# Performance work log

Measured on AMD Instinct MI355X. Metric: run time of the kernel, lower is better.

The kernel has to match this reference:

```python
import jax, jax.numpy as jnp
import numpy as np


def setup_inputs() -> dict:
    key = jax.random.key(0)
    k1, k2, k3, k4, k5 = jax.random.split(key, 5)
    B, S, IC, OC = 4, 2048, 4096, 4096
    n_out = int(0.05 * IC)  # 204 outlier columns
    return {
        "x": jax.random.normal(k1, (B, S, IC), dtype=jnp.float32),
        "weight": jax.random.normal(k2, (OC, IC), dtype=jnp.float32) * 0.02,
        "bias": jax.random.normal(k3, (OC,), dtype=jnp.float32) * 0.02,
        "outlier_weight": jax.random.normal(k4, (OC, n_out), dtype=jnp.float32) * 0.02,
        "outlier_columns_index": jax.random.randint(k5, (n_out,), 0, IC, dtype=jnp.int32),
    }


def reference(x, weight, bias, outlier_weight, outlier_columns_index):
    # XnorBinaryLinear.quant_weight: per-output-row mean-centering,
    # sign binarization, scaled by per-row mean absolute value.
    mean = jnp.mean(weight, axis=1, keepdims=True)            # [OC, 1]
    centered = weight - mean                                  # [OC, IC]
    scale = jnp.mean(jnp.abs(centered), axis=1, keepdims=True)  # [OC, 1]
    q = jnp.sign(centered) * scale                            # binarized weight [OC, IC]
    # scatter fp32 outlier columns back into the binarized weight
    w = q.at[:, outlier_columns_index].set(outlier_weight)    # [OC, IC]
    # F.linear(x, w, bias) = x @ w.T + bias
    out = jnp.einsum('bsi,oi->bso', x, w) + bias
    return out
```

## Files before the change

### kernel.cpp

```cpp
#include <hip/hip_runtime.h>
#include <hip/hip_bf16.h>


typedef __attribute__((ext_vector_type(4))) int i32x4;

__global__ void quant_sign_kernel(const float* __restrict__ w,
                                  const float* __restrict__ ow,
                                  const int* __restrict__ idx,
                                  signed char* __restrict__ qw,
                                  float* __restrict__ sArr,
                                  int IC, int K2, int n_out) {
    __shared__ float red[8];
    __shared__ signed char sgn[4096];
    __shared__ int cmL[4096];
    const int o = blockIdx.x;
    const int t = threadIdx.x;
    const int lane = t & 63, wid = t >> 6;

#pragma unroll
    for (int i = 0; i < 16; ++i) cmL[t + i * 256] = -1;

    const float4* row4 = (const float4*)(w + (size_t)o * IC);
    float4 v[4];
    float s = 0.f;
#pragma unroll
    for (int j = 0; j < 4; ++j) {
        v[j] = row4[t + j * 256];
        s += v[j].x + v[j].y + v[j].z + v[j].w;
    }
#pragma unroll
    for (int off = 32; off; off >>= 1) s += __shfl_down(s, off);
    if (lane == 0) red[wid] = s;
    __syncthreads();
    const float mean = (red[0] + red[1] + red[2] + red[3]) / (float)IC;

    if (t < n_out) atomicMax(&cmL[idx[t]], t);

    float a = 0.f;
#pragma unroll
    for (int j = 0; j < 4; ++j)
        a += fabsf(v[j].x - mean) + fabsf(v[j].y - mean) +
             fabsf(v[j].z - mean) + fabsf(v[j].w - mean);
#pragma unroll
    for (int off = 32; off; off >>= 1) a += __shfl_down(a, off);
    if (lane == 0) red[4 + wid] = a;
    __syncthreads();
    const float scale = (red[4] + red[5] + red[6] + red[7]) / (float)IC;
    if (t == 0) sArr[o] = scale;

    const size_t base = (size_t)o * K2;
#pragma unroll
    for (int j = 0; j < 4; ++j) {
        const int c0 = (t + j * 256) * 4;
        float ee[4] = {v[j].x, v[j].y, v[j].z, v[j].w};
        int pack = 0;
#pragma unroll
        for (int ei = 0; ei < 4; ++ei) {
            float c = ee[ei] - mean;
            int q = c > 0.f ? 8 : (c < 0.f ? -8 : 0);
            pack |= (q & 0xff) << (ei * 8);
        }
        *(int*)(qw + base + c0) = pack;
        *(int*)(sgn + c0) = pack;
    }
    __syncthreads();

    signed char q = 0;
    if (t < n_out) {
        const int c = idx[t];
        if (cmL[c] == t) {
            const float sg = (float)sgn[c] * 0.125f;
            const float wc = ow[(size_t)o * n_out + t] - scale * sg;
            float qf = rintf(8.f * wc / scale);
            qf = fminf(127.f, fmaxf(-127.f, qf));
            q = (signed char)(int)qf;
        }
    }
    qw[base + IC + t] = q;
}

__global__ void quant_x_kernel(const float4* __restrict__ x4,
                               const int* __restrict__ idx,
                               signed char* __restrict__ qx,
                               float* __restrict__ rdel,
                               int IC, int K2, int n_out) {
    __shared__ float red[4];
    __shared__ float bmax;
    __shared__ signed char rowq[4096];
    const int m = blockIdx.x;
    const int t = threadIdx.x;
    const int lane = t & 63, wid = t >> 6;

    const float4* row4 = x4 + (size_t)m * (IC / 4);
    float4 v[4];
    float mx = 0.f;
#pragma unroll
    for (int j = 0; j < 4; ++j) {
        v[j] = row4[t + j * 256];
        mx = fmaxf(mx, fmaxf(fmaxf(fabsf(v[j].x), fabsf(v[j].y)),
                             fmaxf(fabsf(v[j].z), fabsf(v[j].w))));
    }
#pragma unroll
    for (int off = 32; off; off >>= 1) mx = fmaxf(mx, __shfl_down(mx, off));
    if (lane == 0) red[wid] = mx;
    __syncthreads();
    if (t == 0) {
        float m0 = fmaxf(fmaxf(red[0], red[1]), fmaxf(red[2], red[3]));
        bmax = m0;
        rdel[m] = m0 / 127.f;
    }
    __syncthreads();
    const float inv = 127.f / bmax;

    const size_t base = (size_t)m * K2;
#pragma unroll
    for (int j = 0; j < 4; ++j) {
        const int c0 = (t + j * 256) * 4;
        float ee[4] = {v[j].x, v[j].y, v[j].z, v[j].w};
        int pack = 0;
#pragma unroll
        for (int ei = 0; ei < 4; ++ei) {
            int q = (int)rintf(ee[ei] * inv);
            pack |= (q & 0xff) << (ei * 8);
        }
        *(int*)(qx + base + c0) = pack;
        *(int*)(rowq + c0) = pack;
    }
    __syncthreads();

    signed char g = 0;
    if (t < n_out) g = rowq[idx[t]];
    qx[base + IC + t] = g;
}

#define GLDS(src, dst) __builtin_amdgcn_global_load_lds( \
    (const __attribute__((address_space(1))) void*)(src), \
    (__attribute__((address_space(3))) void*)(dst), 16, 0, 0)

#define STAGE64(MAT, bufS, knB) do {                                          \
    const signed char* gsrc_ = (MAT) ? Bblk : Ablk;                           \
    _Pragma("unroll")                                                         \
    for (int rr_ = 0; rr_ < 2; ++rr_) {                                       \
      GLDS(gsrc_ + (size_t)(rr_ * 128 + stg_row) * K2 + (knB) + stg_col,      \
           &ldsb[(bufS) * 32768 + (MAT) * 16384 + (rr_ * 128 + wid * 16) * 64]); \
    } } while (0)

#define RDA(AF, FH, B_) do {                                                  \
    const signed char* pa_ = &ldsb[(B_) * 32768];                             \
    _Pragma("unroll")                                                         \
    for (int j_ = 0; j_ < 4; ++j_)                                            \
      AF[j_] = *(const i32x4*)&pa_[(wr * 128 + ((FH) * 4 + j_) * 16 + l15) * 64 + slB]; \
  } while (0)

#define RDB(BF, B_) do {                                                      \
    const signed char* pb_ = &ldsb[(B_) * 32768 + 16384];                     \
    _Pragma("unroll")                                                         \
    for (int j_ = 0; j_ < 4; ++j_)                                            \
      BF[j_] = *(const i32x4*)&pb_[(wc * 64 + j_ * 16 + l15) * 64 + slB];     \
  } while (0)

#define MM16(FH) do {                                                         \
    _Pragma("unroll")                                                         \
    for (int mi_ = 0; mi_ < 4; ++mi_)                                         \
      _Pragma("unroll")                                                       \
      for (int ni_ = 0; ni_ < 4; ++ni_)                                       \
        acc[(FH) * 4 + mi_][ni_] = __builtin_amdgcn_mfma_i32_16x16x64_i8(     \
            afr[mi_], bfr[ni_], acc[(FH) * 4 + mi_][ni_], 0, 0, 0);           \
  } while (0)

#define KT64(bufR, bufS, knB) do {                                            \
    RDB(bfr, bufR);                                                           \
    RDA(afr, 0, bufR);                                                        \
    STAGE64(0, bufS, knB);                                                    \
    __builtin_amdgcn_s_setprio(1);                                            \
    MM16(0);                                                                  \
    __builtin_amdgcn_s_setprio(0);                                            \
    RDA(afr, 1, bufR);                                                        \
    STAGE64(1, bufS, knB);                                                    \
    asm volatile("s_waitcnt vmcnt(8)" ::: "memory");                          \
    __builtin_amdgcn_s_barrier();                                             \
    __builtin_amdgcn_s_setprio(1);                                            \
    MM16(1);                                                                  \
    __builtin_amdgcn_s_setprio(0);                                            \
    __builtin_amdgcn_s_barrier();                                             \
  } while (0)

__global__ __launch_bounds__(512, 2) void gemm_i8_kernel(
    const signed char* __restrict__ Aq,
    const signed char* __restrict__ Bq,
    const float* __restrict__ bias,
    const float* __restrict__ sArr,
    const float* __restrict__ rdel,
    float* __restrict__ C,
    int M, int N, int K2, int NBN) {
    extern __shared__ signed char ldsb[];

    const int t = threadIdx.x;
    const int wid = t >> 6, lane = t & 63;
    const int l15 = lane & 15;
    const int slB = (((lane >> 4) ^ ((lane >> 1) & 3)) & 3) * 16;
    const int wr = wid >> 2;
    const int wc = wid & 3;
    const int stg_row = wid * 16 + (lane >> 2);
    const int stg_col = (((lane & 3) ^ ((lane >> 3) & 3)) & 3) * 16;

    const int nwg = gridDim.x;
    const int bid = blockIdx.x;
    const int q = nwg >> 3, r = nwg & 7;
    const int xcd = bid & 7, off = bid >> 3;
    const int swz = (xcd < r ? xcd * (q + 1) : r * (q + 1) + (xcd - r) * q) + off;
    const int bm = swz / NBN, bn = swz % NBN;

    const signed char* Ablk = Aq + (size_t)(bm * 256) * K2;
    const signed char* Bblk = Bq + (size_t)(bn * 256) * K2;

    i32x4 acc[8][4] = {};
    i32x4 afr[4], bfr[4];

    STAGE64(0, 0, 0);    STAGE64(1, 0, 0);
    STAGE64(0, 1, 64);   STAGE64(1, 1, 64);
    STAGE64(0, 2, 128);  STAGE64(1, 2, 128);
    asm volatile("s_waitcnt vmcnt(8)" ::: "memory");
    __builtin_amdgcn_s_barrier();

    for (int it = 0; it < 17; ++it) {
        const int tt = it * 4;
        const int k3 = (tt + 3) * 64;
        const int k4 = (tt + 4 < 68) ? (tt + 4) * 64 : 0;
        const int k5 = (tt + 5 < 68) ? (tt + 5) * 64 : 0;
        const int k6 = (tt + 6 < 68) ? (tt + 6) * 64 : 0;
        KT64(0, 3, k3);
        KT64(1, 0, k4);
        KT64(2, 1, k5);
        KT64(3, 2, k6);
    }

    float sv[4], bv[4];
#pragma unroll
    for (int ni = 0; ni < 4; ++ni) {
        const int col = bn * 256 + wc * 64 + ni * 16 + l15;
        sv[ni] = sArr[col] * 0.125f;
        bv[ni] = bias[col];
    }

    const int crow0 = bm * 256 + wr * 128;
    const int ccol = bn * 256 + wc * 64 + l15;
#pragma unroll
    for (int mi = 0; mi < 8; ++mi) {
#pragma unroll
        for (int rr = 0; rr < 4; ++rr) {
            const int row = crow0 + mi * 16 + (lane >> 4) * 4 + rr;
            const float rd = rdel[row];
            float* Crow = C + (size_t)row * N;
#pragma unroll
            for (int ni = 0; ni < 4; ++ni)
                Crow[ccol + ni * 16] =
                    (float)acc[mi][ni][rr] * (sv[ni] * rd) + bv[ni];
        }
    }
}

extern "C" void kernel_launch(void* const* d_in, const int* in_sizes, int n_in,
                              void* d_out, int out_size, void* d_ws, size_t ws_size,
                              hipStream_t stream) {
    const float* x      = (const float*)d_in[0];
    const float* weight = (const float*)d_in[1];
    const float* bias   = (const float*)d_in[2];
    const float* ow     = (const float*)d_in[3];
    const int*   idx    = (const int*)d_in[4];

    const int OC    = in_sizes[2];
    const int n_out = in_sizes[4];
    const int IC    = in_sizes[1] / OC;
    const int M     = in_sizes[0] / IC;
    const int K2    = IC + 256;
    float* out = (float*)d_out;

    char* ws = (char*)d_ws;
    signed char* qx = (signed char*)ws;
    signed char* qw = (signed char*)(ws + (size_t)M * K2);
    float* sArr = (float*)(ws + (size_t)M * K2 + (size_t)OC * K2);
    float* rdel = sArr + OC;

    quant_sign_kernel<<<OC, 256, 0, stream>>>(weight, ow, idx, qw, sArr,
                                              IC, K2, n_out);
    quant_x_kernel<<<M, 256, 0, stream>>>((const float4*)x, idx, qx, rdel,
                                          IC, K2, n_out);

    hipFuncSetAttribute((const void*)gemm_i8_kernel,
                        hipFuncAttributeMaxDynamicSharedMemorySize, 131072);
    const int NBM = M / 256, NBN = OC / 256;
    gemm_i8_kernel<<<dim3(NBM * NBN), dim3(512), 131072, stream>>>(
        qx, qw, bias, sArr, rdel, out, M, OC, K2, NBN);
}
```

Before: 179.5 us.

## Shrink GEMM tile to 128x128 with 256 threads and 3-stage LDS pipeline

Replaces the 256x256 tile, 512-thread int8 GEMM with a 128x128 tile and 256 threads. Each workgroup uses 48KB of LDS in a 3-buffer ring instead of 128KB in 4 buffers, so up to three workgroups can share a CU. The loop restructure adds two tail iterations, and a new XCD-aware mapping gives each XCD a contiguous 32x8 block region for L2 locality. Smaller tiles halve per-block reuse and raise total global and LDS traffic in exchange for more resident waves and more blocks to balance.

```diff
diff --git a/kernel.cpp b/kernel.cpp
--- a/kernel.cpp
+++ b/kernel.cpp
@@ -137,116 +137,114 @@
     (const __attribute__((address_space(1))) void*)(src), \
     (__attribute__((address_space(3))) void*)(dst), 16, 0, 0)
 
-#define STAGE64(MAT, bufS, knB) do {                                          \
-    const signed char* gsrc_ = (MAT) ? Bblk : Ablk;                           \
-    _Pragma("unroll")                                                         \
-    for (int rr_ = 0; rr_ < 2; ++rr_) {                                       \
-      GLDS(gsrc_ + (size_t)(rr_ * 128 + stg_row) * K2 + (knB) + stg_col,      \
-           &ldsb[(bufS) * 32768 + (MAT) * 16384 + (rr_ * 128 + wid * 16) * 64]); \
-    } } while (0)
-
-#define RDA(AF, FH, B_) do {                                                  \
-    const signed char* pa_ = &ldsb[(B_) * 32768];                             \
+#define STG1(MAT, bufS, knB, RR) \
+    GLDS((((MAT) ? Bblk : Ablk) + (size_t)((RR) * 64 + stg_row) * K2 + (knB) + stg_col), \
+         &ldsb[(bufS) * 16384 + (MAT) * 8192 + ((RR) * 64 + wid * 16) * 64])
+
+#define RDA(B_) do {                                                          \
+    const signed char* pa_ = &ldsb[(B_) * 16384];                             \
     _Pragma("unroll")                                                         \
     for (int j_ = 0; j_ < 4; ++j_)                                            \
-      AF[j_] = *(const i32x4*)&pa_[(wr * 128 + ((FH) * 4 + j_) * 16 + l15) * 64 + slB]; \
-  } while (0)
-
-#define RDB(BF, B_) do {                                                      \
-    const signed char* pb_ = &ldsb[(B_) * 32768 + 16384];                     \
+      afr[j_] = *(const i32x4*)&pa_[(wr * 64 + j_ * 16 + l15) * 64 + slB];    \
+  } while (0)
+
+#define RDB(B_) do {                                                          \
+    const signed char* pb_ = &ldsb[(B_) * 16384 + 8192];                      \
     _Pragma("unroll")                                                         \
     for (int j_ = 0; j_ < 4; ++j_)                                            \
-      BF[j_] = *(const i32x4*)&pb_[(wc * 64 + j_ * 16 + l15) * 64 + slB];     \
-  } while (0)
-
-#define MM16(FH) do {                                                         \
+      bfr[j_] = *(const i32x4*)&pb_[(wc * 64 + j_ * 16 + l15) * 64 + slB];    \
+  } while (0)
+
+#define MM16() do {                                                           \
     _Pragma("unroll")                                                         \
     for (int mi_ = 0; mi_ < 4; ++mi_)                                         \
       _Pragma("unroll")                                                       \
       for (int ni_ = 0; ni_ < 4; ++ni_)                                       \
-        acc[(FH) * 4 + mi_][ni_] = __builtin_amdgcn_mfma_i32_16x16x64_i8(     \
-            afr[mi_], bfr[ni_], acc[(FH) * 4 + mi_][ni_], 0, 0, 0);           \
-  } while (0)
-
-#define KT64(bufR, bufS, knB) do {                                            \
-    RDB(bfr, bufR);                                                           \
-    RDA(afr, 0, bufR);                                                        \
-    STAGE64(0, bufS, knB);                                                    \
-    __builtin_amdgcn_s_setprio(1);                                            \
-    MM16(0);                                                                  \
-    __builtin_amdgcn_s_setprio(0);                                            \
-    RDA(afr, 1, bufR);                                                        \
-    STAGE64(1, bufS, knB);                                                    \
-    asm volatile("s_waitcnt vmcnt(8)" ::: "memory");                          \
+        acc[mi_][ni_] = __builtin_amdgcn_mfma_i32_16x16x64_i8(                \
+            afr[mi_], bfr[ni_], acc[mi_][ni_], 0, 0, 0);                      \
+  } while (0)
+
+#define KT(bufR, bufS, knB) do {                                              \
+    RDB(bufR);                                                                \
+    RDA(bufR);                                                                \
+    STG1(0, bufS, knB, 0); STG1(0, bufS, knB, 1);                             \
+    STG1(1, bufS, knB, 0); STG1(1, bufS, knB, 1);                             \
+    asm volatile("s_waitcnt vmcnt(4)" ::: "memory");                          \
     __builtin_amdgcn_s_barrier();                                             \
     __builtin_amdgcn_s_setprio(1);                                            \
-    MM16(1);                                                                  \
+    MM16();                                                                   \
     __builtin_amdgcn_s_setprio(0);                                            \
     __builtin_amdgcn_s_barrier();                                             \
   } while (0)
 
-__global__ __launch_bounds__(512, 2) void gemm_i8_kernel(
+__global__ __launch_bounds__(256, 3) void gemm_i8_kernel(
     const signed char* __restrict__ Aq,
     const signed char* __restrict__ Bq,
     const float* __restrict__ bias,
     const float* __restrict__ sArr,
     const float* __restrict__ rdel,
     float* __restrict__ C,
-    int M, int N, int K2, int NBN) {
+    int M, int N, int K2, int NBM, int NBN) {
     extern __shared__ signed char ldsb[];
 
     const int t = threadIdx.x;
     const int wid = t >> 6, lane = t & 63;
     const int l15 = lane & 15;
     const int slB = (((lane >> 4) ^ ((lane >> 1) & 3)) & 3) * 16;
-    const int wr = wid >> 2;
-    const int wc = wid & 3;
+    const int wr = wid >> 1;
+    const int wc = wid & 1;
     const int stg_row = wid * 16 + (lane >> 2);
     const int stg_col = (((lane & 3) ^ ((lane >> 3) & 3)) & 3) * 16;
 
-    const int nwg = gridDim.x;
     const int bid = blockIdx.x;
-    const int q = nwg >> 3, r = nwg & 7;
-    const int xcd = bid & 7, off = bid >> 3;
-    const int swz = (xcd < r ? xcd * (q + 1) : r * (q + 1) + (xcd - r) * q) + off;
-    const int bm = swz / NBN, bn = swz % NBN;
-
-    const signed char* Ablk = Aq + (size_t)(bm * 256) * K2;
-    const signed char* Bblk = Bq + (size_t)(bn * 256) * K2;
-
-    i32x4 acc[8][4] = {};
+    int bm, bn;
+    if ((NBM & 31) == 0 && (NBN & 7) == 0 && (NBM >> 5) * (NBN >> 3) == 8) {
+        const int xcd = bid & 7, loc = bid >> 3;
+        bm = (xcd >> 2) * 32 + (loc >> 3);
+        bn = (xcd & 3) * 8 + (loc & 7);
+    } else {
+        const int nwg = gridDim.x;
+        const int q = nwg >> 3, r = nwg & 7;
+        const int xcd = bid & 7, off = bid >> 3;
+        const int swz = (xcd < r ? xcd * (q + 1) : r * (q + 1) + (xcd - r) * q) + off;
+        bm = swz / NBN; bn = swz % NBN;
+    }
+
+    const signed char* Ablk = Aq + (size_t)(bm * 128) * K2;
+    const signed char* Bblk = Bq + (size_t)(bn * 128) * K2;
+
+    i32x4 acc[4][4] = {};
     i32x4 afr[4], bfr[4];
 
-    STAGE64(0, 0, 0);    STAGE64(1, 0, 0);
-    STAGE64(0, 1, 64);   STAGE64(1, 1, 64);
-    STAGE64(0, 2, 128);  STAGE64(1, 2, 128);
-    asm volatile("s_waitcnt vmcnt(8)" ::: "memory");
+    STG1(0, 0, 0, 0);  STG1(0, 0, 0, 1);  STG1(1, 0, 0, 0);  STG1(1, 0, 0, 1);
+    STG1(0, 1, 64, 0); STG1(0, 1, 64, 1); STG1(1, 1, 64, 0); STG1(1, 1, 64, 1);
+    asm volatile("s_waitcnt vmcnt(4)" ::: "memory");
     __builtin_amdgcn_s_barrier();
 
-    for (int it = 0; it < 17; ++it) {
-        const int tt = it * 4;
-        const int k3 = (tt + 3) * 64;
-        const int k4 = (tt + 4 < 68) ? (tt + 4) * 64 : 0;
-        const int k5 = (tt + 5 < 68) ? (tt + 5) * 64 : 0;
-        const int k6 = (tt + 6 < 68) ? (tt + 6) * 64 : 0;
-        KT64(0, 3, k3);
-        KT64(1, 0, k4);
-        KT64(2, 1, k5);
-        KT64(3, 2, k6);
-    }
+    for (int it = 0; it < 22; ++it) {
+        const int tt = it * 3;
+        const int ka = (tt + 2) * 64;
+        const int kb = (tt + 3 < 68) ? (tt + 3) * 64 : 0;
+        const int kc = (tt + 4 < 68) ? (tt + 4) * 64 : 0;
+        KT(0, 2, ka);
+        KT(1, 0, kb);
+        KT(2, 1, kc);
+    }
+    KT(0, 2, 0);
+    KT(1, 0, 0);
 
     float sv[4], bv[4];
 #pragma unroll
     for (int ni = 0; ni < 4; ++ni) {
-        const int col = bn * 256 + wc * 64 + ni * 16 + l15;
+        const int col = bn * 128 + wc * 64 + ni * 16 + l15;
         sv[ni] = sArr[col] * 0.125f;
         bv[ni] = bias[col];
     }
 
-    const int crow0 = bm * 256 + wr * 128;
-    const int ccol = bn * 256 + wc * 64 + l15;
-#pragma unroll
-    for (int mi = 0; mi < 8; ++mi) {
+    const int crow0 = bm * 128 + wr * 64;
+    const int ccol = bn * 128 + wc * 64 + l15;
+#pragma unroll
+    for (int mi = 0; mi < 4; ++mi) {
 #pragma unroll
         for (int rr = 0; rr < 4; ++rr) {
             const int row = crow0 + mi * 16 + (lane >> 4) * 4 + rr;
@@ -288,8 +286,8 @@
                                           IC, K2, n_out);
 
     hipFuncSetAttribute((const void*)gemm_i8_kernel,
-                        hipFuncAttributeMaxDynamicSharedMemorySize, 131072);
-    const int NBM = M / 256, NBN = OC / 256;
-    gemm_i8_kernel<<<dim3(NBM * NBN), dim3(512), 131072, stream>>>(
-        qx, qw, bias, sArr, rdel, out, M, OC, K2, NBN);
-}
+                        hipFuncAttributeMaxDynamicSharedMemorySize, 49152);
+    const int NBM = M / 128, NBN = OC / 128;
+    gemm_i8_kernel<<<dim3(NBM * NBN), dim3(256), 49152, stream>>>(
+        qx, qw, bias, sArr, rdel, out, M, OC, K2, NBM, NBN);
+}
```

New measurement: 221.4 us. 23.3% more time.
